# Kernel tuning notes

Measured on AMD Instinct MI355X. Metric: run time of the kernel, lower is better.

Reference implementation:

```python
import jax, jax.numpy as jnp
import numpy as np
import math

B, T, D, H = 16, 256, 1024, 1024
SEG = 16              # segment_len
S = T // SEG          # number of cached segment slots (max_cached_segments=None)
SCALE = 1.0 / math.sqrt(H)


def _ln(x, g, b, eps=1e-5):
    m = jnp.mean(x, -1, keepdims=True)
    v = jnp.mean((x - m) ** 2, -1, keepdims=True)
    return (x - m) * jax.lax.rsqrt(v + eps) * g + b


def _lstm_cell(inp, h, c, Wih, Whh, bih, bhh):
    z = inp @ Wih.T + bih + h @ Whh.T + bhh
    i, f, g, o = jnp.split(z, 4, axis=-1)  # torch LSTMCell gate order i,f,g,o
    c2 = jax.nn.sigmoid(f) * c + jax.nn.sigmoid(i) * jnp.tanh(g)
    return jax.nn.sigmoid(o) * jnp.tanh(c2), c2


def setup_inputs() -> dict:
    key = jax.random.key(0)
    it = iter(jax.random.split(key, 40))

    def un(shape, fan):
        lim = 1.0 / np.sqrt(fan)
        return jax.random.uniform(next(it), shape, jnp.float32, -lim, lim)

    inp = {}
    inp['x'] = jax.random.normal(next(it), (B, T, D), jnp.float32)
    inp['W_ip'] = un((D, D), D); inp['b_ip'] = un((D,), D)
    inp['g_ip'] = jnp.ones((D,), jnp.float32); inp['be_ip'] = jnp.zeros((D,), jnp.float32)
    inp['W_ih0'] = un((4 * H, D), H); inp['W_hh0'] = un((4 * H, H), H)
    inp['b_ih0'] = un((4 * H,), H); inp['b_hh0'] = un((4 * H,), H)
    inp['W_ih1'] = un((4 * H, H), H); inp['W_hh1'] = un((4 * H, H), H)
    inp['b_ih1'] = un((4 * H,), H); inp['b_hh1'] = un((4 * H,), H)
    inp['Wq'] = un((H, H), H); inp['Wk'] = un((H, H), H); inp['Wv'] = un((H, H), H)
    inp['Wg1'] = un((H, 3 * H), 3 * H); inp['bg1'] = un((H,), 3 * H)
    inp['Wg2'] = un((H, H), H); inp['bg2'] = un((H,), H)
    inp['Wo'] = un((H, H), H); inp['bo'] = un((H,), H)
    inp['Wf'] = un((H, 2 * H), 2 * H); inp['bf'] = un((H,), 2 * H)
    inp['g_f'] = jnp.ones((H,), jnp.float32); inp['be_f'] = jnp.zeros((H,), jnp.float32)
    return inp


def reference(x, W_ip, b_ip, g_ip, be_ip,
              W_ih0, W_hh0, b_ih0, b_hh0,
              W_ih1, W_hh1, b_ih1, b_hh1,
              Wq, Wk, Wv, Wg1, bg1, Wg2, bg2, Wo, bo,
              Wf, bf, g_f, be_f):
    # input_proj (eval mode: dropout = identity)
    xp = jax.nn.relu(_ln(x @ W_ip.T + b_ip, g_ip, be_ip))      # [B,T,D]
    xseg = xp.transpose(1, 0, 2).reshape(S, SEG, B, D)          # [S,SEG,B,D]

    def seg_body(carry, xs):
        h0, c0, h1, c1, kbank, vbank = carry
        x_s, s = xs                                             # x_s:[SEG,B,D], s = #cached segments
        valid = jnp.arange(S) < s

        def step(inner, xt):
            h0, c0, h1, c1, seg_sum = inner
            h0, c0 = _lstm_cell(xt, h0, c0, W_ih0, W_hh0, b_ih0, b_hh0)
            h1, c1 = _lstm_cell(h0, h1, c1, W_ih1, W_hh1, b_ih1, b_hh1)
            # SegmentMemoryRetriever, cache_mode='gated_residual'
            q = h1 @ Wq.T
            scores = jnp.einsum('bh,sbh->bs', q, kbank) * SCALE
            scores = jnp.where(valid[None, :], scores, -1e9)
            attn = jax.nn.softmax(scores, axis=-1)
            retrieved = jnp.einsum('bs,sbh->bh', attn, vbank)
            gi = jnp.concatenate([h1, retrieved, h1 - retrieved], -1)
            gate = jax.nn.sigmoid(jax.nn.relu(gi @ Wg1.T + bg1) @ Wg2.T + bg2)
            out = (gate * h1 + (1.0 - gate) * retrieved) @ Wo.T + bo
            ret = jnp.where(s > 0, out, jnp.zeros_like(out))    # empty cache -> zero retrieval
            enh = jax.nn.relu(_ln(jnp.concatenate([h1, ret], -1) @ Wf.T + bf, g_f, be_f))
            return (h0, c0, h1, c1, seg_sum + h1), enh

        init = (h0, c0, h1, c1, jnp.zeros_like(h1))
        (h0, c0, h1, c1, seg_sum), enh = jax.lax.scan(step, init, x_s)
        # append segment to cache; keys/values projected once (linear, equivalent)
        kbank = kbank.at[s].set((seg_sum / SEG) @ Wk.T)         # context = segment mean (use_segment_context)
        vbank = vbank.at[s].set(h1 @ Wv.T)                      # memory = last top hidden of segment
        return (h0, c0, h1, c1, kbank, vbank), enh

    z = jnp.zeros((B, H), x.dtype)
    bank = jnp.zeros((S, B, H), x.dtype)
    carry0 = (z, z, z, z, bank, bank)
    _, enh = jax.lax.scan(seg_body, carry0, (xseg, jnp.arange(S)))
    return enh.reshape(T, B, H).transpose(1, 0, 2)              # sequence_output [B,T,H]
```

## Files before the change

kernel.cpp:

```cpp
#include <hip/hip_runtime.h>
#include <hip/hip_bf16.h>
#include <math.h>

#define B_ 16
#define T_ 256
#define D_ 1024
#define H_ 1024
#define S_ 16
#define SCALE_ (1.0f/32.0f)

typedef __attribute__((ext_vector_type(8))) short short8v;
typedef __attribute__((ext_vector_type(4))) float f32x4;

__device__ __forceinline__ float sigm(float x) { return 1.f / (1.f + expf(-x)); }

__device__ __forceinline__ ushort f2b(float v) {
  __hip_bfloat16 h = __float2bfloat16(v);
  return *reinterpret_cast<ushort*>(&h);
}
__device__ __forceinline__ float b2f(ushort u) {
  union { unsigned u32; float f; } x; x.u32 = ((unsigned)u) << 16; return x.f;
}

__device__ __forceinline__ void glds16(const void* g, void* l) {
  __builtin_amdgcn_global_load_lds((const __attribute__((address_space(1))) void*)g,
                                   (__attribute__((address_space(3))) void*)l, 16, 0, 0);
}

__device__ __forceinline__ void waitflags64(const int* f, int lane) {
  for (;;) {
    int v = __hip_atomic_load(f + lane, __ATOMIC_RELAXED, __HIP_MEMORY_SCOPE_AGENT);
    if (__all(v != 0)) return;
    __builtin_amdgcn_s_sleep(1);
  }
}

__device__ __forceinline__ void publish_pair(ushort* base, int tid, ushort hb) {
  unsigned hi = (unsigned)__shfl_down((int)hb, 1);
  if (!(tid & 1)) {
    unsigned word = (unsigned)hb | (hi << 16);
    __hip_atomic_exchange((unsigned*)base, word,
                          __ATOMIC_RELAXED, __HIP_MEMORY_SCOPE_AGENT);
  }
}

__device__ __forceinline__ float block_sum256(float v) {
  __shared__ float lds[4];
  #pragma unroll
  for (int off = 32; off; off >>= 1) v += __shfl_down(v, off);
  int w = threadIdx.x >> 6;
  if ((threadIdx.x & 63) == 0) lds[w] = v;
  __syncthreads();
  float r = lds[0] + lds[1] + lds[2] + lds[3];
  __syncthreads();
  return r;
}

#define NJOBS 14
struct CvtJobs {
  const float* src[NJOBS];
  ushort* dst[NJOBS];
  int cum[NJOBS + 1];
};

__global__ __launch_bounds__(256)
void cvt_all(CvtJobs J)
{
  int i = blockIdx.x * 256 + threadIdx.x;
  if (i >= J.cum[NJOBS]) return;
  int j = 0;
  #pragma unroll
  for (int k = 1; k < NJOBS; ++k) j += (i >= J.cum[k]) ? 1 : 0;
  int idx = i - J.cum[j];
  float4 v = ((const float4*)J.src[j])[idx];
  ushort4 o; o.x = f2b(v.x); o.y = f2b(v.y); o.z = f2b(v.z); o.w = f2b(v.w);
  ((ushort4*)J.dst[j])[idx] = o;
}

template<int ACT, int REMAP>
__global__ __launch_bounds__(256)
void gemm_bf16(const ushort* __restrict__ A, const ushort* __restrict__ W,
               const float* __restrict__ bias,
               float* __restrict__ Cf, ushort* __restrict__ Cb,
               int M, int N, int K, float ascale, int ldc,
               const ushort* __restrict__ Hx, const float* __restrict__ Rx,
               const ushort* __restrict__ W2, float ascale2, int msplit)
{
  __shared__ char As[16384];
  __shared__ char Bs[16384];
  const int tid = threadIdx.x;
  const int w = tid >> 6, l = tid & 63;
  const int m0 = blockIdx.y * 128, n0 = blockIdx.x * 128;
  const ushort* __restrict__ Wp = (m0 < msplit) ? W : W2;
  const float asc = (m0 < msplit) ? ascale : ascale2;
  const int wm = w >> 1, wn = w & 1;
  const int srow = l >> 3;
  const int sbyte = ((l & 7) * 16) ^ (srow << 4);
  f32x4 acc[4][4];
  #pragma unroll
  for (int i = 0; i < 4; ++i)
    #pragma unroll
    for (int j = 0; j < 4; ++j) acc[i][j] = (f32x4){0.f, 0.f, 0.f, 0.f};

  for (int k0 = 0; k0 < K; k0 += 64) {
    __syncthreads();
    #pragma unroll
    for (int c = 0; c < 4; ++c) {
      int ca = w * 4 + c;
      int r = ca * 8 + srow;
      glds16((const char*)A + (((size_t)(m0 + r) * K + k0) << 1) + sbyte, As + ca * 1024);
      glds16((const char*)Wp + (((size_t)(n0 + r) * K + k0) << 1) + sbyte, Bs + ca * 1024);
    }
    __syncthreads();
    #pragma unroll
    for (int ks = 0; ks < 2; ++ks) {
      short8v a[4], b[4];
      int qb = ks * 64 + (l >> 4) * 16;
      #pragma unroll
      for (int i = 0; i < 4; ++i) {
        int ra = wm * 64 + i * 16 + (l & 15);
        a[i] = *(const short8v*)(As + ra * 128 + (qb ^ ((ra & 7) << 4)));
        int rb = wn * 64 + i * 16 + (l & 15);
        b[i] = *(const short8v*)(Bs + rb * 128 + (qb ^ ((rb & 7) << 4)));
      }
      #pragma unroll
      for (int i = 0; i < 4; ++i)
        #pragma unroll
        for (int j = 0; j < 4; ++j)
          acc[i][j] = __builtin_amdgcn_mfma_f32_16x16x32_bf16(a[i], b[j], acc[i][j], 0, 0, 0);
    }
  }
  #pragma unroll
  for (int i = 0; i < 4; ++i) {
    #pragma unroll
    for (int j = 0; j < 4; ++j) {
      int n = n0 + wn * 64 + j * 16 + (l & 15);
      float bv = bias ? bias[n] : 0.f;
      #pragma unroll
      for (int q = 0; q < 4; ++q) {
        int m = m0 + wm * 64 + i * 16 + (l >> 4) * 4 + q;
        float v = acc[i][j][q] * asc + bv;
        if (ACT == 1) v = fmaxf(v, 0.f);
        if (ACT == 2) v = sigm(v);
        if (ACT == 3) {
          float gte = sigm(v);
          float h = b2f(Hx[(size_t)m * 1024 + n]);
          float r = Rx[(size_t)m * 1024 + n];
          v = gte * h + (1.f - gte) * r;
        }
        if (ACT == 4) v = (m >= 256) ? v : 0.f;
        size_t off = REMAP ? ((size_t)((m & 255) * 16 + (m >> 8)) * ldc + n)
                           : ((size_t)m * ldc + n);
        if (Cf) Cf[off] = v;
        if (Cb) Cb[off] = f2b(v);
      }
    }
  }
}

__global__ __launch_bounds__(256)
void ln_relu_bf16(const float* __restrict__ X, const float* __restrict__ g,
                  const float* __restrict__ be, ushort* __restrict__ out)
{
  size_t row = blockIdx.x;
  const float4* p = (const float4*)(X + row * 1024);
  int tid = threadIdx.x;
  float4 v = p[tid];
  float s = block_sum256(v.x + v.y + v.z + v.w);
  float mean = s * (1.f / 1024.f);
  float dx = v.x - mean, dy = v.y - mean, dz = v.z - mean, dw = v.w - mean;
  float ss = block_sum256(dx*dx + dy*dy + dz*dz + dw*dw);
  float r = rsqrtf(ss * (1.f / 1024.f) + 1e-5f);
  int c4 = tid * 4;
  ushort4 o;
  o.x = f2b(fmaxf(dx * r * g[c4+0] + be[c4+0], 0.f));
  o.y = f2b(fmaxf(dy * r * g[c4+1] + be[c4+1], 0.f));
  o.z = f2b(fmaxf(dz * r * g[c4+2] + be[c4+2], 0.f));
  o.w = f2b(fmaxf(dw * r * g[c4+3] + be[c4+3], 0.f));
  *(ushort4*)(out + row * 1024 + c4) = o;
}

__global__ __launch_bounds__(256)
void ln_relu_final(const float* __restrict__ F, const float* __restrict__ g,
                   const float* __restrict__ be, float* __restrict__ out)
{
  int row = blockIdx.x;
  int t = row >> 4, b = row & 15;
  const float4* p = (const float4*)(F + (size_t)row * 1024);
  int tid = threadIdx.x;
  float4 v = p[tid];
  float s = block_sum256(v.x + v.y + v.z + v.w);
  float mean = s * (1.f / 1024.f);
  float dx = v.x - mean, dy = v.y - mean, dz = v.z - mean, dw = v.w - mean;
  float ss = block_sum256(dx*dx + dy*dy + dz*dz + dw*dw);
  float r = rsqrtf(ss * (1.f / 1024.f) + 1e-5f);
  int c4 = tid * 4;
  float4 o;
  o.x = fmaxf(dx * r * g[c4+0] + be[c4+0], 0.f);
  o.y = fmaxf(dy * r * g[c4+1] + be[c4+1], 0.f);
  o.z = fmaxf(dz * r * g[c4+2] + be[c4+2], 0.f);
  o.w = fmaxf(dw * r * g[c4+3] + be[c4+3], 0.f);
  ((float4*)(out + ((size_t)b * T_ + t) * 1024))[tid] = o;
}

__global__ __launch_bounds__(512)
void lstm_persistent(const ushort* __restrict__ Z0T,
                     const ushort* __restrict__ whh0,
                     const float* __restrict__ bhh0,
                     const ushort* __restrict__ wih1,
                     const ushort* __restrict__ whh1,
                     const float* __restrict__ bih1,
                     const float* __restrict__ bhh1,
                     ushort* __restrict__ HP,
                     ushort* __restrict__ H1B,
                     const ushort* __restrict__ ZP,
                     float* __restrict__ KSUM,
                     int* flag0,
                     int* flag1)
{
  __shared__ char Ah[65536];
  __shared__ float zs[8][16][16];
  __builtin_amdgcn_fence(__ATOMIC_ACQUIRE, "agent");
  const int tid = threadIdx.x, w = tid >> 6, l = tid & 63;
  const int lm = l & 15, lq = l >> 4;
  const int g = w & 3, kh = w >> 2;
  const int jb = blockIdx.x & 63;
  const int j0 = jb * 16;
  const int eb = tid >> 4, ej = tid & 15, jf = j0 + ej;
  float creg = 0.f;
  float br[4];

  if (blockIdx.x < 64) {
    short8v wreg[16];
    {
      const int n = g * 1024 + j0 + lm;
      const ushort* wb = whh0 + (size_t)n * 1024 + kh * 512 + lq * 8;
      #pragma unroll
      for (int ks = 0; ks < 16; ++ks) wreg[ks] = *(const short8v*)(wb + ks * 32);
    }
    if (tid < 256) {
      #pragma unroll
      for (int gg = 0; gg < 4; ++gg) br[gg] = bhh0[gg * 1024 + jf];
    }
    for (int t = 0; t < T_; ++t) {
      float z0v[4];
      if (tid < 256) {
        const ushort* zp = Z0T + ((size_t)t * 16 + eb) * 4096 + jf;
        #pragma unroll
        for (int gg = 0; gg < 4; ++gg) z0v[gg] = b2f(zp[gg * 1024]);
      }
      if (t > 0) {
        if (w == 0) waitflags64(flag0 + (size_t)t * 64, l);
        __syncthreads();
      }
      const ushort* hin = HP + (size_t)t * 16384;
      #pragma unroll
      for (int it = 0; it < 4; ++it) {
        int g1k = w * 4 + it;
        int kc = g1k * 4 + lq;
        int m = lm ^ (kc & 15);
        glds16(hin + (size_t)m * 1024 + kc * 8, Ah + g1k * 1024);
      }
      __syncthreads();
      {
        f32x4 a0 = {0.f,0.f,0.f,0.f}, a1 = {0.f,0.f,0.f,0.f};
        #pragma unroll
        for (int ks = 0; ks < 16; ks += 2) {
          int kc0 = kh * 64 + ks * 4 + lq;
          int kc1 = kc0 + 4;
          short8v f0 = *(const short8v*)(Ah + kc0 * 256 + ((lm ^ (kc0 & 15)) << 4));
          short8v f1 = *(const short8v*)(Ah + kc1 * 256 + ((lm ^ (kc1 & 15)) << 4));
          a0 = __builtin_amdgcn_mfma_f32_16x16x32_bf16(f0, wreg[ks],     a0, 0, 0, 0);
          a1 = __builtin_amdgcn_mfma_f32_16x16x32_bf16(f1, wreg[ks + 1], a1, 0, 0, 0);
        }
        #pragma unroll
        for (int q = 0; q < 4; ++q) zs[w][lq * 4 + q][lm] = a0[q] + a1[q];
      }
      __syncthreads();
      if (tid < 256) {
        float zi = zs[0][eb][ej] + zs[4][eb][ej] + z0v[0] + br[0];
        float zf = zs[1][eb][ej] + zs[5][eb][ej] + z0v[1] + br[1];
        float zg = zs[2][eb][ej] + zs[6][eb][ej] + z0v[2] + br[2];
        float zo = zs[3][eb][ej] + zs[7][eb][ej] + z0v[3] + br[3];
        float cp = sigm(zf) * creg + sigm(zi) * tanhf(zg);
        creg = cp;
        ushort hb = f2b(sigm(zo) * tanhf(cp));
        publish_pair(HP + (size_t)(t + 1) * 16384 + eb * 1024 + jf, tid, hb);
      }
      __syncthreads();
      if (tid == 0)
        __hip_atomic_store(flag0 + (size_t)(t + 1) * 64 + jb, 1,
                           __ATOMIC_RELAXED, __HIP_MEMORY_SCOPE_AGENT);
    }
  } else {
    short8v wreg[32];
    {
      const int n = g * 1024 + j0 + lm;
      const ushort* wb = (kh ? whh1 : wih1) + (size_t)n * 1024 + lq * 8;
      #pragma unroll
      for (int ks = 0; ks < 32; ++ks) wreg[ks] = *(const short8v*)(wb + ks * 32);
    }
    if (tid < 256) {
      #pragma unroll
      for (int gg = 0; gg < 4; ++gg)
        br[gg] = bih1[gg * 1024 + jf] + bhh1[gg * 1024 + jf];
    }
    float ksr = 0.f;
    for (int t = 0; t < T_; ++t) {
      if (w == 0) waitflags64(flag0 + (size_t)(t + 1) * 64, l);
      __syncthreads();
      const ushort* h0n = HP + (size_t)(t + 1) * 16384;
      #pragma unroll
      for (int it = 0; it < 4; ++it) {
        int g1k = w * 4 + it;
        int kc = g1k * 4 + lq;
        int m = lm ^ (kc & 15);
        glds16(h0n + (size_t)m * 1024 + kc * 8, Ah + g1k * 1024);
      }
      if (w == 1 && t > 0) waitflags64(flag1 + (size_t)(t - 1) * 64, l);
      __syncthreads();
      const ushort* h1p = (t > 0) ? (H1B + (size_t)(t - 1) * 16384) : ZP;
      #pragma unroll
      for (int it = 0; it < 4; ++it) {
        int g1k = 32 + w * 4 + it;
        int kc = g1k * 4 + lq;
        int m = lm ^ (kc & 15);
        glds16(h1p + (size_t)m * 1024 + (kc - 128) * 8, Ah + g1k * 1024);
      }
      __syncthreads();
      {
        f32x4 a0 = {0.f,0.f,0.f,0.f}, a1 = {0.f,0.f,0.f,0.f};
        #pragma unroll
        for (int ks = 0; ks < 32; ks += 2) {
          int kc0 = kh * 128 + ks * 4 + lq;
          int kc1 = kc0 + 4;
          short8v f0 = *(const short8v*)(Ah + kc0 * 256 + ((lm ^ (kc0 & 15)) << 4));
          short8v f1 = *(const short8v*)(Ah + kc1 * 256 + ((lm ^ (kc1 & 15)) << 4));
          a0 = __builtin_amdgcn_mfma_f32_16x16x32_bf16(f0, wreg[ks],     a0, 0, 0, 0);
          a1 = __builtin_amdgcn_mfma_f32_16x16x32_bf16(f1, wreg[ks + 1], a1, 0, 0, 0);
        }
        #pragma unroll
        for (int q = 0; q < 4; ++q) zs[w][lq * 4 + q][lm] = a0[q] + a1[q];
      }
      __syncthreads();
      if (tid < 256) {
        float zi = zs[0][eb][ej] + zs[4][eb][ej] + br[0];
        float zf = zs[1][eb][ej] + zs[5][eb][ej] + br[1];
        float zg = zs[2][eb][ej] + zs[6][eb][ej] + br[2];
        float zo = zs[3][eb][ej] + zs[7][eb][ej] + br[3];
        float cp = sigm(zf) * creg + sigm(zi) * tanhf(zg);
        creg = cp;
        float hv = sigm(zo) * tanhf(cp);
        ksr += hv;
        publish_pair(H1B + (size_t)t * 16384 + eb * 1024 + jf, tid, f2b(hv));
        if ((t & 15) == 15) {
          KSUM[((size_t)(t >> 4) * 16 + eb) * 1024 + jf] = ksr;
          ksr = 0.f;
        }
      }
      __syncthreads();
      if (tid == 0)
        __hip_atomic_store(flag1 + (size_t)t * 64 + jb, 1,
                           __ATOMIC_RELAXED, __HIP_MEMORY_SCOPE_AGENT);
    }
  }
}

__global__ __launch_bounds__(256)
void prep_banks(const float* __restrict__ KSUM, ushort* __restrict__ KSB,
                const ushort* __restrict__ H1B)
{
  int r = blockIdx.x;
  int c4 = threadIdx.x * 4;
  float4 v = *(const float4*)(KSUM + (size_t)r * 1024 + c4);
  ushort4 o; o.x = f2b(v.x); o.y = f2b(v.y); o.z = f2b(v.z); o.w = f2b(v.w);
  *(ushort4*)(KSB + (size_t)r * 1024 + c4) = o;
  int src = (r >> 4) * 256 + 240 + (r & 15);
  *(ushort4*)(KSB + (size_t)(256 + r) * 1024 + c4) =
      *(const ushort4*)(H1B + (size_t)src * 1024 + c4);
}

__global__ __launch_bounds__(256)
void attn_gi_cat(const ushort* __restrict__ Q, const ushort* __restrict__ kbank,
                 const ushort* __restrict__ vbank, const ushort* __restrict__ H1B,
                 float* __restrict__ R, ushort* __restrict__ GI,
                 ushort* __restrict__ CATB)
{
  int row = blockIdx.x;
  int t = row >> 4, b = row & 15;
  int si = t >> 4;
  int tid = threadIdx.x, lane = tid & 63, w = tid >> 6;
  __shared__ float sc[16];
  float4 accv = {0.f, 0.f, 0.f, 0.f};
  if (si > 0) {
    const ushort* q = Q + (size_t)row * 1024;
    for (int s = w; s < si; s += 4) {
      const ushort* kk = kbank + ((size_t)s * 16 + b) * 1024;
      float p = 0.f;
      for (int k = lane; k < 1024; k += 64) p += b2f(q[k]) * b2f(kk[k]);
      #pragma unroll
      for (int off = 32; off; off >>= 1) p += __shfl_down(p, off);
      if (lane == 0) sc[s] = p * SCALE_;
    }
    __syncthreads();
    float mx = -1e30f;
    for (int s = 0; s < si; ++s) mx = fmaxf(mx, sc[s]);
    float den = 0.f;
    for (int s = 0; s < si; ++s) den += expf(sc[s] - mx);
    float inv = 1.f / den;
    for (int s = 0; s < si; ++s) {
      float a = expf(sc[s] - mx) * inv;
      ushort4 vv = *(const ushort4*)(vbank + ((size_t)s * 16 + b) * 1024 + tid * 4);
      accv.x += a * b2f(vv.x); accv.y += a * b2f(vv.y);
      accv.z += a * b2f(vv.z); accv.w += a * b2f(vv.w);
    }
  }
  size_t r = row;
  int c4 = tid * 4;
  ((float4*)(R + r * 1024))[tid] = accv;
  ushort4 h4 = *(const ushort4*)(H1B + r * 1024 + c4);
  *(ushort4*)(GI + r * 3072 + c4) = h4;
  ushort4 rb; rb.x = f2b(accv.x); rb.y = f2b(accv.y);
  rb.z = f2b(accv.z); rb.w = f2b(accv.w);
  *(ushort4*)(GI + r * 3072 + 1024 + c4) = rb;
  ushort4 d;
  d.x = f2b(b2f(h4.x) - accv.x); d.y = f2b(b2f(h4.y) - accv.y);
  d.z = f2b(b2f(h4.z) - accv.z); d.w = f2b(b2f(h4.w) - accv.w);
  *(ushort4*)(GI + r * 3072 + 2048 + c4) = d;
  *(ushort4*)(CATB + r * 2048 + c4) = h4;
}

extern "C" void kernel_launch(void* const* d_in, const int* in_sizes, int n_in,
                              void* d_out, int out_size, void* d_ws, size_t ws_size,
                              hipStream_t stream) {
  const float* x     = (const float*)d_in[0];
  const float* W_ip  = (const float*)d_in[1];
  const float* b_ip  = (const float*)d_in[2];
  const float* g_ip  = (const float*)d_in[3];
  const float* be_ip = (const float*)d_in[4];
  const float* W_ih0 = (const float*)d_in[5];
  const float* W_hh0 = (const float*)d_in[6];
  const float* b_ih0 = (const float*)d_in[7];
  const float* b_hh0 = (const float*)d_in[8];
  const float* W_ih1 = (const float*)d_in[9];
  const float* W_hh1 = (const float*)d_in[10];
  const float* b_ih1 = (const float*)d_in[11];
  const float* b_hh1 = (const float*)d_in[12];
  const float* Wq    = (const float*)d_in[13];
  const float* Wk    = (const float*)d_in[14];
  const float* Wv    = (const float*)d_in[15];
  const float* Wg1   = (const float*)d_in[16];
  const float* bg1   = (const float*)d_in[17];
  const float* Wg2   = (const float*)d_in[18];
  const float* bg2   = (const float*)d_in[19];
  const float* Wo    = (const float*)d_in[20];
  const float* bo    = (const float*)d_in[21];
  const float* Wf    = (const float*)d_in[22];
  const float* bff   = (const float*)d_in[23];
  const float* g_f   = (const float*)d_in[24];
  const float* be_f  = (const float*)d_in[25];
  float* out = (float*)d_out;
  char* ws = (char*)d_ws;
  const size_t MB = (size_t)1 << 20;
  const size_t KB = (size_t)1 << 10;

  ushort* WB = (ushort*)(ws);
  ushort* wipB  = WB;
  ushort* wih0B = WB + 1*1048576;
  ushort* whh0B = WB + 5*1048576;
  ushort* wih1B = WB + 9*1048576;
  ushort* whh1B = WB + 13*1048576;
  ushort* wqB   = WB + 17*1048576;
  ushort* wkB   = WB + 18*1048576;
  ushort* wvB   = WB + 19*1048576;
  ushort* wg1B  = WB + 20*1048576;
  ushort* wg2B  = WB + 23*1048576;
  ushort* woB   = WB + 24*1048576;
  ushort* wfB   = WB + 25*1048576;

  ushort* XB   = (ushort*)(ws + 54 * MB);
  float*  XP   = (float*)(ws + 62 * MB);
  ushort* QB   = (ushort*)(ws + 62 * MB);
  char*   SCR  = ws + 78 * MB;
  ushort* Z0T  = (ushort*)SCR;
  ushort* GIB  = (ushort*)SCR;
  ushort* CATB = (ushort*)(SCR + 24 * MB);
  ushort* G1B  = (ushort*)(SCR + 40 * MB);
  ushort* MIXB = (ushort*)SCR;
  float*  FB   = (float*)SCR;
  ushort* H1B  = (ushort*)(ws + 126 * MB);
  ushort* HP   = (ushort*)(ws + 134 * MB);
  float*  R    = (float*)(ws + 134 * MB);
  char*   ST   = ws + 150 * MB;
  int*    flag0 = (int*)(ST);
  int*    flag1 = (int*)(ST + 68 * KB);
  const ushort* ZPc = (const ushort*)(ST + 132 * KB);
  float*  KSUM = (float*)(ST + 192 * KB);
  ushort* KSB  = (ushort*)(ST + 1216 * KB);
  ushort* KBb  = (ushort*)(ST + 2240 * KB);
  ushort* VBb  = KBb + 256 * 1024;

  hipMemsetAsync(ST, 0, 164 * KB, stream);
  hipMemsetAsync(HP, 0, 32 * KB, stream);

  dim3 blk(256);
  {
    CvtJobs J;
    const float* srcs[NJOBS] = { x, W_ip, W_ih0, W_hh0, W_ih1, W_hh1,
                                 Wq, Wk, Wv, Wg1, Wg2, Wo, Wf, nullptr };
    ushort* dsts[NJOBS] = { XB, wipB, wih0B, whh0B, wih1B, whh1B,
                            wqB, wkB, wvB, wg1B, wg2B, woB, wfB, nullptr };
    int n4[NJOBS] = { 1048576, 262144, 1048576, 1048576, 1048576, 1048576,
                      262144, 262144, 262144, 786432, 262144, 262144,
                      524288, 0 };
    int c = 0;
    for (int j = 0; j < NJOBS; ++j) {
      J.src[j] = srcs[j] ? srcs[j] : x;
      J.dst[j] = dsts[j] ? dsts[j] : XB;
      J.cum[j] = c;
      c += n4[j];
    }
    J.cum[NJOBS] = c;
    cvt_all<<<dim3((c + 255) / 256), blk, 0, stream>>>(J);
  }

  const int BIG = 1 << 30;
  gemm_bf16<0,0><<<dim3(1024/128, 4096/128), blk, 0, stream>>>(
      XB, wipB, b_ip, XP, nullptr, 4096, 1024, 1024, 1.f, 1024,
      nullptr, nullptr, wipB, 1.f, BIG);
  ln_relu_bf16<<<4096, blk, 0, stream>>>(XP, g_ip, be_ip, XB);
  gemm_bf16<0,1><<<dim3(4096/128, 4096/128), blk, 0, stream>>>(
      XB, wih0B, b_ih0, nullptr, Z0T, 4096, 4096, 1024, 1.f, 4096,
      nullptr, nullptr, wih0B, 1.f, BIG);
  {
    void* kargs[] = {
      (void*)&Z0T, (void*)&whh0B, (void*)&b_hh0,
      (void*)&wih1B, (void*)&whh1B, (void*)&b_ih1, (void*)&b_hh1,
      (void*)&HP, (void*)&H1B, (void*)&ZPc, (void*)&KSUM,
      (void*)&flag0, (void*)&flag1
    };
    hipLaunchCooperativeKernel((const void*)lstm_persistent,
                               dim3(128), dim3(512), kargs, 0, stream);
  }
  prep_banks<<<256, blk, 0, stream>>>(KSUM, KSB, H1B);
  gemm_bf16<0,0><<<dim3(1024/128, 512/128), blk, 0, stream>>>(
      KSB, wkB, nullptr, nullptr, KBb, 512, 1024, 1024, 1.f/16.f, 1024,
      nullptr, nullptr, wvB, 1.f, 256);
  gemm_bf16<0,0><<<dim3(1024/128, 4096/128), blk, 0, stream>>>(
      H1B, wqB, nullptr, nullptr, QB, 4096, 1024, 1024, 1.f, 1024,
      nullptr, nullptr, wqB, 1.f, BIG);
  attn_gi_cat<<<4096, blk, 0, stream>>>(QB, KBb, VBb, H1B, R, GIB, CATB);
  gemm_bf16<1,0><<<dim3(1024/128, 4096/128), blk, 0, stream>>>(
      GIB, wg1B, bg1, nullptr, G1B, 4096, 1024, 3072, 1.f, 1024,
      nullptr, nullptr, wg1B, 1.f, BIG);
  gemm_bf16<3,0><<<dim3(1024/128, 4096/128), blk, 0, stream>>>(
      G1B, wg2B, bg2, nullptr, MIXB, 4096, 1024, 1024, 1.f, 1024,
      H1B, R, wg2B, 1.f, BIG);
  gemm_bf16<4,0><<<dim3(1024/128, 4096/128), blk, 0, stream>>>(
      MIXB, woB, bo, nullptr, CATB + 1024, 4096, 1024, 1024, 1.f, 2048,
      nullptr, nullptr, woB, 1.f, BIG);
  gemm_bf16<0,0><<<dim3(1024/128, 4096/128), blk, 0, stream>>>(
      CATB, wfB, bff, FB, nullptr, 4096, 1024, 2048, 1.f, 1024,
      nullptr, nullptr, wfB, 1.f, BIG);
  ln_relu_final<<<4096, blk, 0, stream>>>(FB, g_f, be_f, out);
}
```

Measured before the change: 1.378 ms.

## Reassociate query projection onto key bank and fold Wg1 over h-r

```diff
diff --git a/kernel.cpp b/kernel.cpp
--- a/kernel.cpp
+++ b/kernel.cpp
@@ -56,7 +56,7 @@
   return r;
 }
 
-#define NJOBS 14
+#define NJOBS 12
 struct CvtJobs {
   const float* src[NJOBS];
   ushort* dst[NJOBS];
@@ -77,13 +77,55 @@
   ((ushort4*)J.dst[j])[idx] = o;
 }
 
+__global__ __launch_bounds__(256)
+void tr_cvt(const float* __restrict__ src, ushort* __restrict__ dst)
+{
+  __shared__ float tile[64][65];
+  const int bx = blockIdx.x, by = blockIdx.y;
+  const int tx = threadIdx.x & 15, ty = threadIdx.x >> 4;
+  #pragma unroll
+  for (int p = 0; p < 4; ++p) {
+    int r = p * 16 + ty;
+    float4 v = *(const float4*)(src + (size_t)(by * 64 + r) * 1024 + bx * 64 + tx * 4);
+    tile[r][tx*4+0] = v.x; tile[r][tx*4+1] = v.y;
+    tile[r][tx*4+2] = v.z; tile[r][tx*4+3] = v.w;
+  }
+  __syncthreads();
+  #pragma unroll
+  for (int p = 0; p < 4; ++p) {
+    int c = p * 16 + ty;
+    ushort4 o;
+    o.x = f2b(tile[tx*4+0][c]); o.y = f2b(tile[tx*4+1][c]);
+    o.z = f2b(tile[tx*4+2][c]); o.w = f2b(tile[tx*4+3][c]);
+    *(ushort4*)(dst + (size_t)(bx * 64 + c) * 1024 + by * 64 + tx * 4) = o;
+  }
+}
+
+__global__ __launch_bounds__(256)
+void wg1_fold(const float* __restrict__ Wg1, ushort* __restrict__ dst)
+{
+  int n = blockIdx.x;
+  int c4 = threadIdx.x * 4;
+  const float* row = Wg1 + (size_t)n * 3072;
+  float4 a = *(const float4*)(row + c4);
+  float4 b = *(const float4*)(row + 1024 + c4);
+  float4 c = *(const float4*)(row + 2048 + c4);
+  ushort4 h, r;
+  h.x = f2b(a.x + c.x); h.y = f2b(a.y + c.y);
+  h.z = f2b(a.z + c.z); h.w = f2b(a.w + c.w);
+  r.x = f2b(b.x - c.x); r.y = f2b(b.y - c.y);
+  r.z = f2b(b.z - c.z); r.w = f2b(b.w - c.w);
+  *(ushort4*)(dst + (size_t)n * 2048 + c4) = h;
+  *(ushort4*)(dst + (size_t)n * 2048 + 1024 + c4) = r;
+}
+
 template<int ACT, int REMAP>
 __global__ __launch_bounds__(256)
 void gemm_bf16(const ushort* __restrict__ A, const ushort* __restrict__ W,
                const float* __restrict__ bias,
                float* __restrict__ Cf, ushort* __restrict__ Cb,
                int M, int N, int K, float ascale, int ldc,
-               const ushort* __restrict__ Hx, const float* __restrict__ Rx,
+               const ushort* __restrict__ Hx, const ushort* __restrict__ Rxb,
                const ushort* __restrict__ W2, float ascale2, int msplit)
 {
   __shared__ char As[16384];
@@ -141,11 +183,10 @@
         int m = m0 + wm * 64 + i * 16 + (l >> 4) * 4 + q;
         float v = acc[i][j][q] * asc + bv;
         if (ACT == 1) v = fmaxf(v, 0.f);
-        if (ACT == 2) v = sigm(v);
         if (ACT == 3) {
           float gte = sigm(v);
           float h = b2f(Hx[(size_t)m * 1024 + n]);
-          float r = Rx[(size_t)m * 1024 + n];
+          float r = b2f(Rxb[(size_t)m * 2048 + n]);
           v = gte * h + (1.f - gte) * r;
         }
         if (ACT == 4) v = (m >= 256) ? v : 0.f;
@@ -159,16 +200,16 @@
 }
 
 __global__ __launch_bounds__(256)
-void ln_relu_bf16(const float* __restrict__ X, const float* __restrict__ g,
+void ln_relu_bf16(const ushort* __restrict__ X, const float* __restrict__ g,
                   const float* __restrict__ be, ushort* __restrict__ out)
 {
   size_t row = blockIdx.x;
-  const float4* p = (const float4*)(X + row * 1024);
   int tid = threadIdx.x;
-  float4 v = p[tid];
-  float s = block_sum256(v.x + v.y + v.z + v.w);
+  ushort4 u = *(const ushort4*)(X + row * 1024 + tid * 4);
+  float vx = b2f(u.x), vy = b2f(u.y), vz = b2f(u.z), vw = b2f(u.w);
+  float s = block_sum256(vx + vy + vz + vw);
   float mean = s * (1.f / 1024.f);
-  float dx = v.x - mean, dy = v.y - mean, dz = v.z - mean, dw = v.w - mean;
+  float dx = vx - mean, dy = vy - mean, dz = vz - mean, dw = vw - mean;
   float ss = block_sum256(dx*dx + dy*dy + dz*dz + dw*dw);
   float r = rsqrtf(ss * (1.f / 1024.f) + 1e-5f);
   int c4 = tid * 4;
@@ -381,10 +422,8 @@
 }
 
 __global__ __launch_bounds__(256)
-void attn_gi_cat(const ushort* __restrict__ Q, const ushort* __restrict__ kbank,
-                 const ushort* __restrict__ vbank, const ushort* __restrict__ H1B,
-                 float* __restrict__ R, ushort* __restrict__ GI,
-                 ushort* __restrict__ CATB)
+void attn_rh(const ushort* __restrict__ H1B, const ushort* __restrict__ KKb,
+             const ushort* __restrict__ vbank, ushort* __restrict__ RHB)
 {
   int row = blockIdx.x;
   int t = row >> 4, b = row & 15;
@@ -393,9 +432,9 @@
   __shared__ float sc[16];
   float4 accv = {0.f, 0.f, 0.f, 0.f};
   if (si > 0) {
-    const ushort* q = Q + (size_t)row * 1024;
+    const ushort* q = H1B + (size_t)row * 1024;
     for (int s = w; s < si; s += 4) {
-      const ushort* kk = kbank + ((size_t)s * 16 + b) * 1024;
+      const ushort* kk = KKb + ((size_t)s * 16 + b) * 1024;
       float p = 0.f;
       for (int k = lane; k < 1024; k += 64) p += b2f(q[k]) * b2f(kk[k]);
       #pragma unroll
@@ -417,17 +456,11 @@
   }
   size_t r = row;
   int c4 = tid * 4;
-  ((float4*)(R + r * 1024))[tid] = accv;
   ushort4 h4 = *(const ushort4*)(H1B + r * 1024 + c4);
-  *(ushort4*)(GI + r * 3072 + c4) = h4;
+  *(ushort4*)(RHB + r * 2048 + c4) = h4;
   ushort4 rb; rb.x = f2b(accv.x); rb.y = f2b(accv.y);
   rb.z = f2b(accv.z); rb.w = f2b(accv.w);
-  *(ushort4*)(GI + r * 3072 + 1024 + c4) = rb;
-  ushort4 d;
-  d.x = f2b(b2f(h4.x) - accv.x); d.y = f2b(b2f(h4.y) - accv.y);
-  d.z = f2b(b2f(h4.z) - accv.z); d.w = f2b(b2f(h4.w) - accv.w);
-  *(ushort4*)(GI + r * 3072 + 2048 + c4) = d;
-  *(ushort4*)(CATB + r * 2048 + c4) = h4;
+  *(ushort4*)(RHB + r * 2048 + 1024 + c4) = rb;
 }
 
 extern "C" void kernel_launch(void* const* d_in, const int* in_sizes, int n_in,
@@ -470,27 +503,24 @@
   ushort* whh0B = WB + 5*1048576;
   ushort* wih1B = WB + 9*1048576;
   ushort* whh1B = WB + 13*1048576;
-  ushort* wqB   = WB + 17*1048576;
+  ushort* wqTB  = WB + 17*1048576;
   ushort* wkB   = WB + 18*1048576;
   ushort* wvB   = WB + 19*1048576;
-  ushort* wg1B  = WB + 20*1048576;
+  ushort* wg1F  = WB + 20*1048576;
   ushort* wg2B  = WB + 23*1048576;
   ushort* woB   = WB + 24*1048576;
   ushort* wfB   = WB + 25*1048576;
 
   ushort* XB   = (ushort*)(ws + 54 * MB);
-  float*  XP   = (float*)(ws + 62 * MB);
-  ushort* QB   = (ushort*)(ws + 62 * MB);
+  ushort* XPP  = (ushort*)(ws + 62 * MB);
   char*   SCR  = ws + 78 * MB;
   ushort* Z0T  = (ushort*)SCR;
-  ushort* GIB  = (ushort*)SCR;
-  ushort* CATB = (ushort*)(SCR + 24 * MB);
-  ushort* G1B  = (ushort*)(SCR + 40 * MB);
-  ushort* MIXB = (ushort*)SCR;
-  float*  FB   = (float*)SCR;
+  ushort* RHB  = (ushort*)SCR;
+  ushort* G1B  = (ushort*)(SCR + 16 * MB);
+  ushort* MIXB = (ushort*)(SCR + 24 * MB);
+  float*  FB   = (float*)(SCR + 32 * MB);
   ushort* H1B  = (ushort*)(ws + 126 * MB);
   ushort* HP   = (ushort*)(ws + 134 * MB);
-  float*  R    = (float*)(ws + 134 * MB);
   char*   ST   = ws + 150 * MB;
   int*    flag0 = (int*)(ST);
   int*    flag1 = (int*)(ST + 68 * KB);
@@ -499,6 +529,7 @@
   ushort* KSB  = (ushort*)(ST + 1216 * KB);
   ushort* KBb  = (ushort*)(ST + 2240 * KB);
   ushort* VBb  = KBb + 256 * 1024;
+  ushort* KKb  = (ushort*)(ST + 3264 * KB);
 
   hipMemsetAsync(ST, 0, 164 * KB, stream);
   hipMemsetAsync(HP, 0, 32 * KB, stream);
@@ -507,12 +538,11 @@
   {
     CvtJobs J;
     const float* srcs[NJOBS] = { x, W_ip, W_ih0, W_hh0, W_ih1, W_hh1,
-                                 Wq, Wk, Wv, Wg1, Wg2, Wo, Wf, nullptr };
+                                 Wk, Wv, Wg2, Wo, Wf, nullptr };
     ushort* dsts[NJOBS] = { XB, wipB, wih0B, whh0B, wih1B, whh1B,
-                            wqB, wkB, wvB, wg1B, wg2B, woB, wfB, nullptr };
+                            wkB, wvB, wg2B, woB, wfB, nullptr };
     int n4[NJOBS] = { 1048576, 262144, 1048576, 1048576, 1048576, 1048576,
-                      262144, 262144, 262144, 786432, 262144, 262144,
-                      524288, 0 };
+                      262144, 262144, 262144, 262144, 524288, 0 };
     int c = 0;
     for (int j = 0; j < NJOBS; ++j) {
       J.src[j] = srcs[j] ? srcs[j] : x;
@@ -523,12 +553,14 @@
     J.cum[NJOBS] = c;
     cvt_all<<<dim3((c + 255) / 256), blk, 0, stream>>>(J);
   }
+  tr_cvt<<<dim3(16, 16), blk, 0, stream>>>(Wq, wqTB);
+  wg1_fold<<<1024, blk, 0, stream>>>(Wg1, wg1F);
 
   const int BIG = 1 << 30;
   gemm_bf16<0,0><<<dim3(1024/128, 4096/128), blk, 0, stream>>>(
-      XB, wipB, b_ip, XP, nullptr, 4096, 1024, 1024, 1.f, 1024,
+      XB, wipB, b_ip, nullptr, XPP, 4096, 1024, 1024, 1.f, 1024,
       nullptr, nullptr, wipB, 1.f, BIG);
-  ln_relu_bf16<<<4096, blk, 0, stream>>>(XP, g_ip, be_ip, XB);
+  ln_relu_bf16<<<4096, blk, 0, stream>>>(XPP, g_ip, be_ip, XB);
   gemm_bf16<0,1><<<dim3(4096/128, 4096/128), blk, 0, stream>>>(
       XB, wih0B, b_ih0, nullptr, Z0T, 4096, 4096, 1024, 1.f, 4096,
       nullptr, nullptr, wih0B, 1.f, BIG);
@@ -546,21 +578,21 @@
   gemm_bf16<0,0><<<dim3(1024/128, 512/128), blk, 0, stream>>>(
       KSB, wkB, nullptr, nullptr, KBb, 512, 1024, 1024, 1.f/16.f, 1024,
       nullptr, nullptr, wvB, 1.f, 256);
-  gemm_bf16<0,0><<<dim3(1024/128, 4096/128), blk, 0, stream>>>(
-      H1B, wqB, nullptr, nullptr, QB, 4096, 1024, 1024, 1.f, 1024,
-      nullptr, nullptr, wqB, 1.f, BIG);
-  attn_gi_cat<<<4096, blk, 0, stream>>>(QB, KBb, VBb, H1B, R, GIB, CATB);
+  gemm_bf16<0,0><<<dim3(1024/128, 256/128), blk, 0, stream>>>(
+      KBb, wqTB, nullptr, nullptr, KKb, 256, 1024, 1024, 1.f, 1024,
+      nullptr, nullptr, wqTB, 1.f, BIG);
+  attn_rh<<<4096, blk, 0, stream>>>(H1B, KKb, VBb, RHB);
   gemm_bf16<1,0><<<dim3(1024/128, 4096/128), blk, 0, stream>>>(
-      GIB, wg1B, bg1, nullptr, G1B, 4096, 1024, 3072, 1.f, 1024,
-      nullptr, nullptr, wg1B, 1.f, BIG);
+      RHB, wg1F, bg1, nullptr, G1B, 4096, 1024, 2048, 1.f, 1024,
+      nullptr, nullptr, wg1F, 1.f, BIG);
   gemm_bf16<3,0><<<dim3(1024/128, 4096/128), blk, 0, stream>>>(
       G1B, wg2B, bg2, nullptr, MIXB, 4096, 1024, 1024, 1.f, 1024,
-      H1B, R, wg2B, 1.f, BIG);
+      H1B, RHB + 1024, wg2B, 1.f, BIG);
   gemm_bf16<4,0><<<dim3(1024/128, 4096/128), blk, 0, stream>>>(
-      MIXB, woB, bo, nullptr, CATB + 1024, 4096, 1024, 1024, 1.f, 2048,
+      MIXB, woB, bo, nullptr, RHB + 1024, 4096, 1024, 1024, 1.f, 2048,
       nullptr, nullptr, woB, 1.f, BIG);
   gemm_bf16<0,0><<<dim3(1024/128, 4096/128), blk, 0, stream>>>(
-      CATB, wfB, bff, FB, nullptr, 4096, 1024, 2048, 1.f, 1024,
+      RHB, wfB, bff, FB, nullptr, 4096, 1024, 2048, 1.f, 1024,
       nullptr, nullptr, wfB, 1.f, BIG);
   ln_relu_final<<<4096, blk, 0, stream>>>(FB, g_f, be_f, out);
 }
```

Result: no change. 1.358 ms (median of 2 runs) (-1.4%).
